# Performance work log

Hardware: AMD Instinct MI355X
Metric: run time of the kernel (lower is better)

Reference implementation:

```python
import jax, jax.numpy as jnp
import numpy as np

N_NODES = 50000
N_EDGES = 800000
C_IN = 128
HID = 128
C_OUT = 128


def _glorot(key, shape):
    fan_in, fan_out = shape
    lim = (6.0 / (fan_in + fan_out)) ** 0.5
    return jax.random.uniform(key, shape, jnp.float32, -lim, lim)


def setup_inputs() -> dict:
    key = jax.random.key(0)
    ks = jax.random.split(key, 8)
    x = jax.random.normal(ks[0], (N_NODES, C_IN), jnp.float32)
    edge_index = jax.random.randint(ks[1], (2, N_EDGES), 0, N_NODES, jnp.int32)
    return {
        "x": x,
        "edge_index": edge_index,
        # nn_in: Lin(2*C_IN, HID) -> ReLU -> Lin(HID, HID)
        "W1_in": _glorot(ks[2], (2 * C_IN, HID)), "b1_in": jnp.zeros((HID,), jnp.float32),
        "W2_in": _glorot(ks[3], (HID, HID)), "b2_in": jnp.zeros((HID,), jnp.float32),
        # nn_hid: Lin(2*HID, HID) -> ReLU -> Lin(HID, HID)
        "W1_hid": _glorot(ks[4], (2 * HID, HID)), "b1_hid": jnp.zeros((HID,), jnp.float32),
        "W2_hid": _glorot(ks[5], (HID, HID)), "b2_hid": jnp.zeros((HID,), jnp.float32),
        # nn_out: Lin(2*HID, HID) -> ReLU -> Lin(HID, C_OUT)
        "W1_out": _glorot(ks[6], (2 * HID, HID)), "b1_out": jnp.zeros((HID,), jnp.float32),
        "W2_out": _glorot(ks[7], (HID, C_OUT)), "b2_out": jnp.zeros((C_OUT,), jnp.float32),
    }


def _edge_conv(x, src, dst, W1, b1, W2, b2, n_nodes):
    # PyG EdgeConv: message = nn(concat(x_i, x_j - x_i)), aggr='max' over incoming edges
    xi = x[dst]                                   # [E, C] destination (center) nodes
    xj = x[src]                                   # [E, C] source (neighbor) nodes
    m = jnp.concatenate([xi, xj - xi], axis=-1)   # [E, 2C]
    h = jax.nn.relu(m @ W1 + b1) @ W2 + b2        # [E, H]
    agg = jax.ops.segment_max(h, dst, num_segments=n_nodes)  # [N, H]
    # PyG fills nodes with no incoming edges with 0 (segment_max yields -inf)
    return jnp.where(jnp.isfinite(agg), agg, 0.0)


def reference(x, edge_index, W1_in, b1_in, W2_in, b2_in,
              W1_hid, b1_hid, W2_hid, b2_hid,
              W1_out, b1_out, W2_out, b2_out):
    src, dst = edge_index[0], edge_index[1]
    n = x.shape[0]
    x = _edge_conv(x, src, dst, W1_in, b1_in, W2_in, b2_in, n)
    x = jax.nn.relu(x)
    x = _edge_conv(x, src, dst, W1_hid, b1_hid, W2_hid, b2_hid, n)
    x = jax.nn.relu(x)
    x = _edge_conv(x, src, dst, W1_out, b1_out, W2_out, b2_out, n)
    return x
```

## Files before the change

kernel.cpp:

```cpp
#include <hip/hip_runtime.h>

#define CH 128
#define NPB 16

typedef _Float16 f16;
typedef _Float16 f16x8 __attribute__((ext_vector_type(8)));
typedef float f32x4 __attribute__((ext_vector_type(4)));

__device__ __forceinline__ f32x4 mfma16(f16x8 a, f16x8 b, f32x4 c) {
    return __builtin_amdgcn_mfma_f32_16x16x32_f16(a, b, c, 0, 0, 0);
}

__global__ __launch_bounds__(256) void k_front(const int* __restrict__ edst, int* __restrict__ counts, int E,
                                               const float* __restrict__ W1a, const float* __restrict__ W2a,
                                               const float* __restrict__ W1b, const float* __restrict__ W2b,
                                               const float* __restrict__ W1c, const float* __restrict__ W2c,
                                               f16* __restrict__ WcT, f16* __restrict__ W2T,
                                               const float* __restrict__ x, f16* __restrict__ act,
                                               int total4, int gHist) {
    int bid = blockIdx.x;
    if (bid < gHist) {
        int e = bid * 256 + threadIdx.x;
        if (e < E) atomicAdd(&counts[edst[e]], 1);
    } else if (bid < gHist + 576) {
        int r = bid - gHist;
        int l = r / 192;
        const float* W1 = (l == 0) ? W1a : (l == 1) ? W1b : W1c;
        const float* W2 = (l == 0) ? W2a : (l == 1) ? W2b : W2c;
        f16* wct = WcT + l * 256 * CH;
        f16* w2t = W2T + l * CH * CH;
        int id = (r % 192) * 256 + threadIdx.x;
        if (id < 32768) {
            int n = id >> 7, k = id & 127;
            float v;
            if (n < CH) v = W1[k * CH + n] - W1[(CH + k) * CH + n];
            else        v = W1[(CH + k) * CH + (n - CH)];
            wct[n * CH + k] = (f16)v;
        } else {
            int rr = id - 32768;
            int n = rr >> 7, k = rr & 127;
            w2t[n * CH + k] = (f16)W2[k * CH + n];
        }
    } else {
        int i = (bid - gHist - 576) * 256 + threadIdx.x;
        if (i < total4) {
            float4 v = ((const float4*)x)[i];
            f16 h0 = (f16)v.x, h1 = (f16)v.y, h2 = (f16)v.z, h3 = (f16)v.w;
            short4 s;
            s.x = *(short*)&h0; s.y = *(short*)&h1; s.z = *(short*)&h2; s.w = *(short*)&h3;
            ((short4*)act)[i] = s;
        }
    }
}

__global__ __launch_bounds__(256) void k_scan1(const int* __restrict__ counts, int* __restrict__ row_ptr,
                                               int* __restrict__ blockSums, int n) {
    __shared__ int s[256];
    int t = threadIdx.x;
    int i = blockIdx.x * 256 + t;
    s[t] = (i < n) ? counts[i] : 0;
    __syncthreads();
    for (int off = 1; off < 256; off <<= 1) {
        int x = (t >= off) ? s[t - off] : 0;
        __syncthreads();
        s[t] += x;
        __syncthreads();
    }
    if (i < n) row_ptr[i + 1] = s[t];
    if (t == 255) blockSums[blockIdx.x] = s[255];
}

__global__ __launch_bounds__(256) void k_scan2(const int* __restrict__ blockSums, int* __restrict__ blockOff, int nb) {
    __shared__ int s[256];
    int t = threadIdx.x;
    s[t] = (t < nb) ? blockSums[t] : 0;
    __syncthreads();
    for (int off = 1; off < 256; off <<= 1) {
        int x = (t >= off) ? s[t - off] : 0;
        __syncthreads();
        s[t] += x;
        __syncthreads();
    }
    blockOff[t] = (t == 0) ? 0 : s[t - 1];
}

__global__ __launch_bounds__(256) void k_scan3(int* __restrict__ row_ptr, const int* __restrict__ blockOff, int n) {
    int i = blockIdx.x * 256 + threadIdx.x;
    if (i < n) row_ptr[i + 1] += blockOff[blockIdx.x];
    if (blockIdx.x == 0 && threadIdx.x == 0) row_ptr[0] = 0;
}

__global__ __launch_bounds__(256) void k_scatter(const int* __restrict__ src, const int* __restrict__ dst,
                                                 const int* __restrict__ row_ptr, int* __restrict__ cursor,
                                                 int2* __restrict__ sed, int E) {
    int e = blockIdx.x * 256 + threadIdx.x;
    if (e < E) {
        int d = dst[e];
        int pos = row_ptr[d] + atomicAdd(&cursor[d], 1);
        sed[pos] = make_int2(src[e], d);
    }
}

__global__ __launch_bounds__(256) void k_gemm1(const f16* __restrict__ act, const f16* __restrict__ WcT,
                                               const float* __restrict__ b1,
                                               f16* __restrict__ P, f16* __restrict__ Q, int nrows) {
    int t = threadIdx.x;
    int w = t >> 6, lane = t & 63;
    int m = lane & 15, q = lane >> 4;
    int rowbase = blockIdx.x * 256 + w * 64;
    f16x8 a[4][4];
#pragma unroll
    for (int rt = 0; rt < 4; ++rt) {
        int rowc = min(rowbase + rt * 16 + m, nrows - 1);
#pragma unroll
        for (int kk = 0; kk < 4; ++kk)
            a[rt][kk] = *(const f16x8*)(act + (size_t)rowc * CH + kk * 32 + q * 8);
    }
#pragma unroll
    for (int nb = 0; nb < 16; ++nb) {
        f16x8 b[4];
#pragma unroll
        for (int kk = 0; kk < 4; ++kk)
            b[kk] = *(const f16x8*)(WcT + (nb * 16 + m) * CH + kk * 32 + q * 8);
        int col = nb * 16 + m;
        float bias = (nb < 8) ? b1[col] : 0.f;
#pragma unroll
        for (int rt = 0; rt < 4; ++rt) {
            f32x4 acc = {0.f, 0.f, 0.f, 0.f};
#pragma unroll
            for (int kk = 0; kk < 4; ++kk) acc = mfma16(a[rt][kk], b[kk], acc);
#pragma unroll
            for (int r = 0; r < 4; ++r) {
                int ro = rowbase + rt * 16 + q * 4 + r;
                if (ro < nrows) {
                    float v = acc[r] + bias;
                    if (nb < 8) P[(size_t)ro * CH + col] = (f16)v;
                    else        Q[(size_t)ro * CH + (col - CH)] = (f16)v;
                }
            }
        }
    }
}

__global__ __launch_bounds__(256) void k_edge(const f16* __restrict__ P, const f16* __restrict__ Q,
                                              const f16* __restrict__ W2Tg, const float* __restrict__ b2,
                                              const int* __restrict__ row_ptr, const int2* __restrict__ sed,
                                              f16* __restrict__ act_out, float* __restrict__ final_out,
                                              int n_nodes, int flags) {
    __shared__ __align__(16) f16 buf[2][32 * 136];
    __shared__ unsigned char ndrel[2][32];
    __shared__ unsigned accs[NPB * CH];

    int t = threadIdx.x;
    int w = t >> 6, lane = t & 63;
    int m1 = lane & 15, q1 = lane >> 4;
    int mp = t >> 4, c = t & 15;
    int n0 = blockIdx.x * NPB;
    const f16x8 z8 = {};

#pragma unroll
    for (int i = t; i < NPB * CH; i += 256) accs[i] = 0u;

    int rs = row_ptr[min(n0, n_nodes)];
    int re = row_ptr[min(n0 + NPB, n_nodes)];
    int ntiles = (re - rs + 31) >> 5;

    f16x8 bf[2][4];
#pragma unroll
    for (int i2 = 0; i2 < 2; ++i2)
#pragma unroll
        for (int kk = 0; kk < 4; ++kk)
            bf[i2][kk] = *(const f16x8*)(W2Tg + ((2 * w + i2) * 16 + m1) * CH + kk * 32 + q1 * 8);

    auto flip = [](float x) -> unsigned {
        unsigned u = __float_as_uint(x);
        return u ^ (0x80000000u | (unsigned)((int)u >> 31));
    };

    auto consume = [&](int par) {
#pragma unroll
        for (int rt = 0; rt < 2; ++rt) {
            f16x8 af[4];
#pragma unroll
            for (int kk = 0; kk < 4; ++kk)
                af[kk] = *(const f16x8*)&buf[par][(rt * 16 + m1) * 136 + kk * 32 + q1 * 8];
            unsigned nid4 = *(const unsigned*)&ndrel[par][rt * 16 + q1 * 4];
            unsigned b0 = nid4 & 255u;
            bool uni = (nid4 == b0 * 0x01010101u);
#pragma unroll
            for (int i2 = 0; i2 < 2; ++i2) {
                f32x4 a = {0.f, 0.f, 0.f, 0.f};
#pragma unroll
                for (int kk = 0; kk < 4; ++kk) a = mfma16(af[kk], bf[i2][kk], a);
                int col = (2 * w + i2) * 16 + m1;
                if (uni) {
                    float m = fmaxf(fmaxf(a[0], a[1]), fmaxf(a[2], a[3]));
                    atomicMax(&accs[b0 * CH + col], flip(m));
                } else {
#pragma unroll
                    for (int r = 0; r < 4; ++r) {
                        int node = (nid4 >> (8 * r)) & 255;
                        atomicMax(&accs[node * CH + col], flip(a[r]));
                    }
                }
            }
        }
    };

    if (ntiles > 0) {
        int2 ia0, ib0, ia1, ib1;
        f16x8 qa0, pa0, qb0, pb0, qa1, pa1, qb1, pb1;

        auto loadIdx = [&](int tt, int2& ia, int2& ib) {
            int e0 = rs + tt * 32;
            ia = sed[min(e0 + mp, re - 1)];
            ib = sed[min(e0 + 16 + mp, re - 1)];
        };
        auto loadData = [&](int2 ia, int2 ib,
                            f16x8& qa, f16x8& pa, f16x8& qb, f16x8& pb) {
            qa = *(const f16x8*)(Q + (size_t)ia.x * CH + c * 8);
            pa = *(const f16x8*)(P + (size_t)ia.y * CH + c * 8);
            qb = *(const f16x8*)(Q + (size_t)ib.x * CH + c * 8);
            pb = *(const f16x8*)(P + (size_t)ib.y * CH + c * 8);
        };
        auto produce = [&](int par, f16x8 qa, f16x8 pa, f16x8 qb, f16x8 pb, int da, int db) {
            *(f16x8*)&buf[par][mp * 136 + c * 8]        = __builtin_elementwise_max(pa + qa, z8);
            *(f16x8*)&buf[par][(16 + mp) * 136 + c * 8] = __builtin_elementwise_max(pb + qb, z8);
            if (c == 0) {
                ndrel[par][mp]      = (unsigned char)(da - n0);
                ndrel[par][16 + mp] = (unsigned char)(db - n0);
            }
        };

        loadIdx(0, ia0, ib0);
        loadData(ia0, ib0, qa0, pa0, qb0, pb0);
        produce(0, qa0, pa0, qb0, pb0, ia0.y, ib0.y);
        if (ntiles > 1) {
            loadIdx(1, ia1, ib1);
            loadData(ia1, ib1, qa1, pa1, qb1, pb1);
        }
        if (ntiles > 2) loadIdx(2, ia0, ib0);
        __syncthreads();

        auto step = [&](int i, int par,
                        f16x8& pqa, f16x8& ppa, f16x8& pqb, f16x8& ppb, int pda, int pdb,
                        f16x8& nqa, f16x8& npa, f16x8& nqb, f16x8& npb,
                        int2 i2a, int2 i2b,
                        int2& i3a, int2& i3b) {
            if (i + 3 < ntiles) loadIdx(i + 3, i3a, i3b);
            if (i + 2 < ntiles) loadData(i2a, i2b, nqa, npa, nqb, npb);
            consume(par);
            if (i + 1 < ntiles) produce(par ^ 1, pqa, ppa, pqb, ppb, pda, pdb);
            __syncthreads();
        };

        int i = 0;
        while (i < ntiles) {
            step(i, 0, qa1, pa1, qb1, pb1, ia1.y, ib1.y, qa0, pa0, qb0, pb0,
                 ia0, ib0, ia1, ib1); ++i;
            if (i >= ntiles) break;
            step(i, 1, qa0, pa0, qb0, pb0, ia0.y, ib0.y, qa1, pa1, qb1, pb1,
                 ia1, ib1, ia0, ib0); ++i;
        }
    }
    __syncthreads();

#pragma unroll
    for (int j = 0; j < NPB * CH / 256; ++j) {
        int idx = t + j * 256;
        int node = idx >> 7, col = idx & 127;
        int gn = n0 + node;
        if (gn < n_nodes) {
            unsigned u = accs[idx];
            float o = 0.f;
            if (u != 0u) {
                float v = (u & 0x80000000u) ? __uint_as_float(u & 0x7FFFFFFFu)
                                            : __uint_as_float(~u);
                o = v + b2[col];
                if (flags & 1) o = fmaxf(o, 0.f);
            }
            if (flags & 2) final_out[(size_t)gn * CH + col] = o;
            else           act_out[(size_t)gn * CH + col] = (f16)o;
        }
    }
}

extern "C" void kernel_launch(void* const* d_in, const int* in_sizes, int n_in,
                              void* d_out, int out_size, void* d_ws, size_t ws_size,
                              hipStream_t stream) {
    const float* x = (const float*)d_in[0];
    const int* ei  = (const int*)d_in[1];
    int E = in_sizes[1] / 2;
    int N = in_sizes[0] / CH;
    const int* esrc = ei;
    const int* edst = ei + E;

    const float* W1[3] = {(const float*)d_in[2], (const float*)d_in[6],  (const float*)d_in[10]};
    const float* B1[3] = {(const float*)d_in[3], (const float*)d_in[7],  (const float*)d_in[11]};
    const float* W2[3] = {(const float*)d_in[4], (const float*)d_in[8],  (const float*)d_in[12]};
    const float* B2[3] = {(const float*)d_in[5], (const float*)d_in[9],  (const float*)d_in[13]};

    char* base = (char*)d_ws;
    size_t off = 0;
    auto alloc = [&](size_t bytes) -> void* {
        void* p = base + off;
        off = (off + bytes + 255) & ~(size_t)255;
        return p;
    };
    int* counts    = (int*)alloc(sizeof(int) * (size_t)(N + 256));
    int* cursor    = (int*)alloc(sizeof(int) * (size_t)(N + 256));
    size_t zero_bytes = off;
    int* row_ptr   = (int*)alloc(sizeof(int) * (size_t)(N + 1));
    int* blockSums = (int*)alloc(sizeof(int) * 256);
    int* blockOff  = (int*)alloc(sizeof(int) * 256);
    int2* sed      = (int2*)alloc(sizeof(int2) * (size_t)E);
    f16* act       = (f16*)alloc(sizeof(f16) * (size_t)N * CH);
    f16* Pb        = (f16*)alloc(sizeof(f16) * (size_t)N * CH);
    f16* Qb        = (f16*)alloc(sizeof(f16) * (size_t)N * CH);
    f16* WcT       = (f16*)alloc(sizeof(f16) * 3 * 256 * CH);
    f16* W2T       = (f16*)alloc(sizeof(f16) * 3 * CH * CH);

    hipMemsetAsync(d_ws, 0, zero_bytes, stream);

    int gE = (E + 255) / 256;
    int gN = (N + 255) / 256;
    int total4 = N * CH / 4;
    int gCvt = (total4 + 255) / 256;
    k_front<<<gE + 576 + gCvt, 256, 0, stream>>>(edst, counts, E,
                                                 W1[0], W2[0], W1[1], W2[1], W1[2], W2[2],
                                                 WcT, W2T, x, act, total4, gE);
    k_scan1<<<gN, 256, 0, stream>>>(counts, row_ptr, blockSums, N);
    k_scan2<<<1, 256, 0, stream>>>(blockSums, blockOff, gN);
    k_scan3<<<gN, 256, 0, stream>>>(row_ptr, blockOff, N);
    k_scatter<<<gE, 256, 0, stream>>>(esrc, edst, row_ptr, cursor, sed, E);

    int gEdge = (N + NPB - 1) / NPB;
    int gG1 = (N + 255) / 256;
    for (int l = 0; l < 3; ++l) {
        k_gemm1<<<gG1, 256, 0, stream>>>(act, WcT + l * 256 * CH, B1[l], Pb, Qb, N);
        int flags = (l < 2) ? 1 : 2;
        k_edge<<<gEdge, 256, 0, stream>>>(Pb, Qb, W2T + l * CH * CH, B2[l],
                                          row_ptr, sed, act, (float*)d_out, N, flags);
    }
}
```

Before: 443.1 us.

## Replace tiled edge kernel with wave-per-node kernel keeping max in registers

The block-of-16-nodes edge kernel, with its LDS staging, double buffering and shared-memory atomicMax aggregation, is replaced by a persistent kernel in which each wave owns one destination node at a time. The wave holds the whole W2 tile and the node's P row in registers, gathers 16 source Q rows per step, runs MFMAs over all 128 output columns, and keeps a running max in registers. A cross-lane shuffle reduction then replaces the LDS atomics and the block barriers. The sorted edge list now stores only the source index, halving its size. The cost is higher register pressure, and low-degree nodes leave most of the 16 MFMA rows empty.

New measurement: 535.0 us. 1.21x slower.

```diff
diff --git a/kernel.cpp b/kernel.cpp
--- a/kernel.cpp
+++ b/kernel.cpp
@@ -1,7 +1,6 @@
 #include <hip/hip_runtime.h>
 
 #define CH 128
-#define NPB 16
 
 typedef _Float16 f16;
 typedef _Float16 f16x8 __attribute__((ext_vector_type(8)));
@@ -92,12 +91,12 @@
 
 __global__ __launch_bounds__(256) void k_scatter(const int* __restrict__ src, const int* __restrict__ dst,
                                                  const int* __restrict__ row_ptr, int* __restrict__ cursor,
-                                                 int2* __restrict__ sed, int E) {
+                                                 int* __restrict__ sed, int E) {
     int e = blockIdx.x * 256 + threadIdx.x;
     if (e < E) {
         int d = dst[e];
         int pos = row_ptr[d] + atomicAdd(&cursor[d], 1);
-        sed[pos] = make_int2(src[e], d);
+        sed[pos] = src[e];
     }
 }
 
@@ -142,145 +141,90 @@
     }
 }
 
-__global__ __launch_bounds__(256) void k_edge(const f16* __restrict__ P, const f16* __restrict__ Q,
-                                              const f16* __restrict__ W2Tg, const float* __restrict__ b2,
-                                              const int* __restrict__ row_ptr, const int2* __restrict__ sed,
-                                              f16* __restrict__ act_out, float* __restrict__ final_out,
-                                              int n_nodes, int flags) {
-    __shared__ __align__(16) f16 buf[2][32 * 136];
-    __shared__ unsigned char ndrel[2][32];
-    __shared__ unsigned accs[NPB * CH];
-
+__global__ __launch_bounds__(256, 2)
+void k_node(const f16* __restrict__ P, const f16* __restrict__ Q,
+            const f16* __restrict__ W2Tg, const float* __restrict__ b2,
+            const int* __restrict__ row_ptr, const int* __restrict__ sed,
+            f16* __restrict__ act_out, float* __restrict__ final_out,
+            int n_nodes, int flags, int nwaves) {
     int t = threadIdx.x;
     int w = t >> 6, lane = t & 63;
-    int m1 = lane & 15, q1 = lane >> 4;
-    int mp = t >> 4, c = t & 15;
-    int n0 = blockIdx.x * NPB;
+    int m = lane & 15, q = lane >> 4;
+
+    f16x8 bf[8][4];
+#pragma unroll
+    for (int nb = 0; nb < 8; ++nb)
+#pragma unroll
+        for (int kk = 0; kk < 4; ++kk)
+            bf[nb][kk] = *(const f16x8*)(W2Tg + (size_t)(nb * 16 + m) * CH + kk * 32 + q * 8);
+
+    float biasA = b2[lane], biasB = b2[lane + 64];
     const f16x8 z8 = {};
-
-#pragma unroll
-    for (int i = t; i < NPB * CH; i += 256) accs[i] = 0u;
-
-    int rs = row_ptr[min(n0, n_nodes)];
-    int re = row_ptr[min(n0 + NPB, n_nodes)];
-    int ntiles = (re - rs + 31) >> 5;
-
-    f16x8 bf[2][4];
-#pragma unroll
-    for (int i2 = 0; i2 < 2; ++i2)
-#pragma unroll
-        for (int kk = 0; kk < 4; ++kk)
-            bf[i2][kk] = *(const f16x8*)(W2Tg + ((2 * w + i2) * 16 + m1) * CH + kk * 32 + q1 * 8);
-
-    auto flip = [](float x) -> unsigned {
-        unsigned u = __float_as_uint(x);
-        return u ^ (0x80000000u | (unsigned)((int)u >> 31));
-    };
-
-    auto consume = [&](int par) {
-#pragma unroll
-        for (int rt = 0; rt < 2; ++rt) {
-            f16x8 af[4];
+    const f32x4 z4 = {0.f, 0.f, 0.f, 0.f};
+
+    for (int node = blockIdx.x * 4 + w; node < n_nodes; node += nwaves) {
+        int rs = row_ptr[node];
+        int re = row_ptr[node + 1];
+
+        float o0 = 0.f, o1 = 0.f;
+        if (re > rs) {
+            const f16* prow = P + (size_t)node * CH;
+            f16x8 pf[4];
 #pragma unroll
             for (int kk = 0; kk < 4; ++kk)
-                af[kk] = *(const f16x8*)&buf[par][(rt * 16 + m1) * 136 + kk * 32 + q1 * 8];
-            unsigned nid4 = *(const unsigned*)&ndrel[par][rt * 16 + q1 * 4];
-            unsigned b0 = nid4 & 255u;
-            bool uni = (nid4 == b0 * 0x01010101u);
-#pragma unroll
-            for (int i2 = 0; i2 < 2; ++i2) {
-                f32x4 a = {0.f, 0.f, 0.f, 0.f};
-#pragma unroll
-                for (int kk = 0; kk < 4; ++kk) a = mfma16(af[kk], bf[i2][kk], a);
-                int col = (2 * w + i2) * 16 + m1;
-                if (uni) {
-                    float m = fmaxf(fmaxf(a[0], a[1]), fmaxf(a[2], a[3]));
-                    atomicMax(&accs[b0 * CH + col], flip(m));
-                } else {
-#pragma unroll
-                    for (int r = 0; r < 4; ++r) {
-                        int node = (nid4 >> (8 * r)) & 255;
-                        atomicMax(&accs[node * CH + col], flip(a[r]));
-                    }
+                pf[kk] = *(const f16x8*)(prow + kk * 32 + q * 8);
+
+            float rmax[8];
+#pragma unroll
+            for (int nb = 0; nb < 8; ++nb) rmax[nb] = -3.4e38f;
+
+            int sNext = sed[min(rs + m, re - 1)];
+            for (int tb = rs; tb < re; tb += 16) {
+                int s = sNext;
+                if (tb + 16 < re) sNext = sed[min(tb + 16 + m, re - 1)];
+
+                const f16* qrow = Q + (size_t)s * CH;
+                f16x8 qs[4];
+#pragma unroll
+                for (int kk = 0; kk < 4; ++kk)
+                    qs[kk] = *(const f16x8*)(qrow + kk * 32 + q * 8);
+
+                f32x4 acc[8];
+                {
+                    f16x8 af = __builtin_elementwise_max(pf[0] + qs[0], z8);
+#pragma unroll
+                    for (int nb = 0; nb < 8; ++nb) acc[nb] = mfma16(af, bf[nb][0], z4);
                 }
+#pragma unroll
+                for (int kk = 1; kk < 4; ++kk) {
+                    f16x8 af = __builtin_elementwise_max(pf[kk] + qs[kk], z8);
+#pragma unroll
+                    for (int nb = 0; nb < 8; ++nb) acc[nb] = mfma16(af, bf[nb][kk], acc[nb]);
+                }
+#pragma unroll
+                for (int nb = 0; nb < 8; ++nb)
+                    rmax[nb] = fmaxf(fmaxf(fmaxf(acc[nb][0], acc[nb][1]),
+                                           fmaxf(acc[nb][2], acc[nb][3])), rmax[nb]);
             }
-        }
-    };
-
-    if (ntiles > 0) {
-        int2 ia0, ib0, ia1, ib1;
-        f16x8 qa0, pa0, qb0, pb0, qa1, pa1, qb1, pb1;
-
-        auto loadIdx = [&](int tt, int2& ia, int2& ib) {
-            int e0 = rs + tt * 32;
-            ia = sed[min(e0 + mp, re - 1)];
-            ib = sed[min(e0 + 16 + mp, re - 1)];
-        };
-        auto loadData = [&](int2 ia, int2 ib,
-                            f16x8& qa, f16x8& pa, f16x8& qb, f16x8& pb) {
-            qa = *(const f16x8*)(Q + (size_t)ia.x * CH + c * 8);
-            pa = *(const f16x8*)(P + (size_t)ia.y * CH + c * 8);
-            qb = *(const f16x8*)(Q + (size_t)ib.x * CH + c * 8);
-            pb = *(const f16x8*)(P + (size_t)ib.y * CH + c * 8);
-        };
-        auto produce = [&](int par, f16x8 qa, f16x8 pa, f16x8 qb, f16x8 pb, int da, int db) {
-            *(f16x8*)&buf[par][mp * 136 + c * 8]        = __builtin_elementwise_max(pa + qa, z8);
-            *(f16x8*)&buf[par][(16 + mp) * 136 + c * 8] = __builtin_elementwise_max(pb + qb, z8);
-            if (c == 0) {
-                ndrel[par][mp]      = (unsigned char)(da - n0);
-                ndrel[par][16 + mp] = (unsigned char)(db - n0);
+#pragma unroll
+            for (int nb = 0; nb < 8; ++nb) {
+                float v = rmax[nb];
+                v = fmaxf(v, __shfl_xor(v, 16));
+                v = fmaxf(v, __shfl_xor(v, 32));
+                rmax[nb] = v;
             }
-        };
-
-        loadIdx(0, ia0, ib0);
-        loadData(ia0, ib0, qa0, pa0, qb0, pb0);
-        produce(0, qa0, pa0, qb0, pb0, ia0.y, ib0.y);
-        if (ntiles > 1) {
-            loadIdx(1, ia1, ib1);
-            loadData(ia1, ib1, qa1, pa1, qb1, pb1);
-        }
-        if (ntiles > 2) loadIdx(2, ia0, ib0);
-        __syncthreads();
-
-        auto step = [&](int i, int par,
-                        f16x8& pqa, f16x8& ppa, f16x8& pqb, f16x8& ppb, int pda, int pdb,
-                        f16x8& nqa, f16x8& npa, f16x8& nqb, f16x8& npb,
-                        int2 i2a, int2 i2b,
-                        int2& i3a, int2& i3b) {
-            if (i + 3 < ntiles) loadIdx(i + 3, i3a, i3b);
-            if (i + 2 < ntiles) loadData(i2a, i2b, nqa, npa, nqb, npb);
-            consume(par);
-            if (i + 1 < ntiles) produce(par ^ 1, pqa, ppa, pqb, ppb, pda, pdb);
-            __syncthreads();
-        };
-
-        int i = 0;
-        while (i < ntiles) {
-            step(i, 0, qa1, pa1, qb1, pb1, ia1.y, ib1.y, qa0, pa0, qb0, pb0,
-                 ia0, ib0, ia1, ib1); ++i;
-            if (i >= ntiles) break;
-            step(i, 1, qa0, pa0, qb0, pb0, ia0.y, ib0.y, qa1, pa1, qb1, pb1,
-                 ia1, ib1, ia0, ib0); ++i;
-        }
-    }
-    __syncthreads();
-
-#pragma unroll
-    for (int j = 0; j < NPB * CH / 256; ++j) {
-        int idx = t + j * 256;
-        int node = idx >> 7, col = idx & 127;
-        int gn = n0 + node;
-        if (gn < n_nodes) {
-            unsigned u = accs[idx];
-            float o = 0.f;
-            if (u != 0u) {
-                float v = (u & 0x80000000u) ? __uint_as_float(u & 0x7FFFFFFFu)
-                                            : __uint_as_float(~u);
-                o = v + b2[col];
-                if (flags & 1) o = fmaxf(o, 0.f);
-            }
-            if (flags & 2) final_out[(size_t)gn * CH + col] = o;
-            else           act_out[(size_t)gn * CH + col] = (f16)o;
+            float vA = (q & 2) ? ((q & 1) ? rmax[3] : rmax[2]) : ((q & 1) ? rmax[1] : rmax[0]);
+            float vB = (q & 2) ? ((q & 1) ? rmax[7] : rmax[6]) : ((q & 1) ? rmax[5] : rmax[4]);
+            o0 = vA + biasA;
+            o1 = vB + biasB;
+            if (flags & 1) { o0 = fmaxf(o0, 0.f); o1 = fmaxf(o1, 0.f); }
+        }
+        if (flags & 2) {
+            float* orow = final_out + (size_t)node * CH;
+            orow[lane] = o0; orow[lane + 64] = o1;
+        } else {
+            f16* orow = act_out + (size_t)node * CH;
+            orow[lane] = (f16)o0; orow[lane + 64] = (f16)o1;
         }
     }
 }
@@ -313,7 +257,7 @@
     int* row_ptr   = (int*)alloc(sizeof(int) * (size_t)(N + 1));
     int* blockSums = (int*)alloc(sizeof(int) * 256);
     int* blockOff  = (int*)alloc(sizeof(int) * 256);
-    int2* sed      = (int2*)alloc(sizeof(int2) * (size_t)E);
+    int* sed       = (int*)alloc(sizeof(int) * (size_t)E);
     f16* act       = (f16*)alloc(sizeof(f16) * (size_t)N * CH);
     f16* Pb        = (f16*)alloc(sizeof(f16) * (size_t)N * CH);
     f16* Qb        = (f16*)alloc(sizeof(f16) * (size_t)N * CH);
@@ -334,12 +278,14 @@
     k_scan3<<<gN, 256, 0, stream>>>(row_ptr, blockOff, N);
     k_scatter<<<gE, 256, 0, stream>>>(esrc, edst, row_ptr, cursor, sed, E);
 
-    int gEdge = (N + NPB - 1) / NPB;
+    int gNode = 2048;
+    if (gNode > (N + 3) / 4) gNode = (N + 3) / 4;
+    int nwv = gNode * 4;
     int gG1 = (N + 255) / 256;
     for (int l = 0; l < 3; ++l) {
         k_gemm1<<<gG1, 256, 0, stream>>>(act, WcT + l * 256 * CH, B1[l], Pb, Qb, N);
         int flags = (l < 2) ? 1 : 2;
-        k_edge<<<gEdge, 256, 0, stream>>>(Pb, Qb, W2T + l * CH * CH, B2[l],
-                                          row_ptr, sed, act, (float*)d_out, N, flags);
-    }
-}
+        k_node<<<gNode, 256, 0, stream>>>(Pb, Qb, W2T + l * CH * CH, B2[l],
+                                          row_ptr, sed, act, (float*)d_out, N, flags, nwv);
+    }
+}
```
